# Performance work log

Measured on AMD Instinct MI355X. Metric: run time of the kernel, lower is better.

The kernel has to match this reference:

```python
import jax, jax.numpy as jnp
import numpy as np

FORGET_BIAS = 1.0  # TF BasicLSTMCell default


def lstm_scan(xs, kernel, bias, init_c, init_h):
    """xs: [T, B, D_in]; kernel: [D_in+H, 4H] with TF gate order i, j, f, o."""
    def step(carry, x):
        c, h = carry
        z = jnp.concatenate([x, h], axis=-1) @ kernel + bias  # [B, 4H]
        i, j, f, o = jnp.split(z, 4, axis=-1)
        c_new = c * jax.nn.sigmoid(f + FORGET_BIAS) + jax.nn.sigmoid(i) * jnp.tanh(j)
        h_new = jnp.tanh(c_new) * jax.nn.sigmoid(o)
        return (c_new, h_new), h_new

    (c, h), hs = jax.lax.scan(step, (init_c, init_h), xs)
    return hs, (c, h)


def setup_inputs() -> dict:
    key = jax.random.key(0)
    ks = jax.random.split(key, 8)
    B, T, F = 128, 32, 2048
    H, L, WV, V = 1024, 20, 300, 10000
    s_enc = 1.0 / np.sqrt(F + H)
    s_dec = 1.0 / np.sqrt(WV + H)
    s_prj = 1.0 / np.sqrt(H)
    return {
        "frames": jax.random.normal(ks[0], (B, T, F), jnp.float32),
        "caption": jax.random.randint(ks[1], (B, L), 0, V, jnp.int32),
        "embeddings": jax.random.normal(ks[2], (V, WV), jnp.float32),
        "enc_kernel": jax.random.normal(ks[3], (F + H, 4 * H), jnp.float32) * s_enc,
        "enc_bias": jnp.zeros((4 * H,), jnp.float32),
        "dec_kernel": jax.random.normal(ks[4], (WV + H, 4 * H), jnp.float32) * s_dec,
        "dec_bias": jnp.zeros((4 * H,), jnp.float32),
        "proj_W": jax.random.normal(ks[5], (H, WV), jnp.float32) * s_prj,
        "proj_b": jnp.zeros((WV,), jnp.float32),
    }


def reference(frames, caption, embeddings, enc_kernel, enc_bias,
              dec_kernel, dec_bias, proj_W, proj_b):
    B = frames.shape[0]
    H = proj_W.shape[0]
    # ----- encoder LSTM over video frames -----
    init = (jnp.zeros((B, H), frames.dtype), jnp.zeros((B, H), frames.dtype))
    xs = jnp.swapaxes(frames, 0, 1)  # [T, B, F]
    _, enc_state = lstm_scan(xs, enc_kernel, enc_bias, *init)

    # ----- decoder LSTM with teacher forcing (training branch) -----
    cap_emb = embeddings[caption]                 # [B, L, WV]
    dec_in = jnp.swapaxes(cap_emb, 0, 1)          # [L, B, WV]
    hs, _ = lstm_scan(dec_in, dec_kernel, dec_bias, *enc_state)  # [L, B, H]
    preds = hs @ proj_W + proj_b                  # [L, B, WV]
    return jnp.swapaxes(preds, 0, 1)              # [B, L, WV]
```

## Files before the change

### kernel.cpp

```cpp
#include <hip/hip_runtime.h>
#include <math.h>

#define B_ 128
#define T_ 32
#define F_ 2048
#define H_ 1024
#define L_ 20
#define WV_ 300
#define WVP_ 320
#define NPJ_ 384

typedef unsigned short u16;
typedef unsigned int u32;
typedef __attribute__((ext_vector_type(8))) short bf16x8;
typedef __attribute__((ext_vector_type(4))) float f32x4;

__device__ __forceinline__ u16 f2bf(float x) {
    union { float f; u32 u; } v; v.f = x;
    return (u16)((v.u + 0x7FFFu + ((v.u >> 16) & 1u)) >> 16);
}
__device__ __forceinline__ float bf2f(u16 x) {
    union { u32 u; float f; } v; v.u = ((u32)x) << 16; return v.f;
}
__device__ __forceinline__ void split3(float x, u16& h, u16& m, u16& l) {
    h = f2bf(x);  float r1 = x - bf2f(h);
    m = f2bf(r1); float r2 = r1 - bf2f(m);
    l = f2bf(r2);
}
__device__ __forceinline__ float sigf(float x) { return 1.0f / (1.0f + expf(-x)); }

__device__ __forceinline__ void g2lds16(const void* g, void* l) {
    __builtin_amdgcn_global_load_lds((const __attribute__((address_space(1))) void*)g,
                                     (__attribute__((address_space(3))) void*)l, 16, 0, 0);
}

__device__ __forceinline__ bf16x8 fragld(const u16* tile, int rbase, int lane) {
    int r = rbase + (lane & 15);
    int byte = r * 64 + ((((lane >> 4) ^ (r >> 1)) & 3) << 4);
    return *(const bf16x8*)((const char*)tile + byte);
}

__device__ __forceinline__ void stage_tile(const u16* src, int row_stride, int k0,
                                           u16* lds, int s) {
    int row = s >> 2;
    int ch = (s & 3) ^ ((row >> 1) & 3);
    g2lds16(src + (size_t)row * row_stride + k0 + ch * 8, lds + (size_t)s * 8);
}

template<int MODE_C>
__global__ __launch_bounds__(256)
void gemm6_tn(int M, int N, int K, int Nreal, int NB,
              const u16* __restrict__ A, int lda, size_t aps,
              const u16* __restrict__ Bt, int ldb, size_t bps,
              const float* __restrict__ bias, float* __restrict__ C, int ldc)
{
    __shared__ u16 As[2][3][128 * 32];
    __shared__ u16 Bs[2][3][128 * 32];
    const int tid = threadIdx.x, lane = tid & 63, wid = tid >> 6;
    const int wr = wid >> 1, wc = wid & 1;
    const int bid = blockIdx.x;
    const int bm = (bid / NB) * 128, bn = (bid % NB) * 128;

    f32x4 acc[4][4] = {};
    const u16* Ar = A + (size_t)bm * lda;
    const u16* Br = Bt + (size_t)bn * ldb;

    auto STAGE = [&](int bsel, int k0) {
#pragma unroll
        for (int p = 0; p < 3; ++p) {
            stage_tile(Ar + p * aps, lda, k0, (u16*)As[bsel][p], tid);
            stage_tile(Ar + p * aps, lda, k0, (u16*)As[bsel][p], tid + 256);
            stage_tile(Br + p * bps, ldb, k0, (u16*)Bs[bsel][p], tid);
            stage_tile(Br + p * bps, ldb, k0, (u16*)Bs[bsel][p], tid + 256);
        }
    };

    const int KT = K >> 5;
    STAGE(0, 0);
    __syncthreads();
    for (int kt = 0; kt < KT; ++kt) {
        int pb = kt & 1;
        if (kt + 1 < KT) STAGE(pb ^ 1, (kt + 1) << 5);
        bf16x8 af[3][4];
#pragma unroll
        for (int p = 0; p < 3; ++p)
#pragma unroll
            for (int m = 0; m < 4; ++m) af[p][m] = fragld(As[pb][p], wr * 64 + m * 16, lane);
        {
            bf16x8 bf[4];
#pragma unroll
            for (int n = 0; n < 4; ++n) bf[n] = fragld(Bs[pb][2], wc * 64 + n * 16, lane);
#pragma unroll
            for (int m = 0; m < 4; ++m)
#pragma unroll
                for (int n = 0; n < 4; ++n)
                    acc[m][n] = __builtin_amdgcn_mfma_f32_16x16x32_bf16(af[0][m], bf[n], acc[m][n], 0, 0, 0);
        }
        {
            bf16x8 bf[4];
#pragma unroll
            for (int n = 0; n < 4; ++n) bf[n] = fragld(Bs[pb][1], wc * 64 + n * 16, lane);
#pragma unroll
            for (int m = 0; m < 4; ++m)
#pragma unroll
                for (int n = 0; n < 4; ++n)
                    acc[m][n] = __builtin_amdgcn_mfma_f32_16x16x32_bf16(af[1][m], bf[n], acc[m][n], 0, 0, 0);
#pragma unroll
            for (int m = 0; m < 4; ++m)
#pragma unroll
                for (int n = 0; n < 4; ++n)
                    acc[m][n] = __builtin_amdgcn_mfma_f32_16x16x32_bf16(af[0][m], bf[n], acc[m][n], 0, 0, 0);
        }
        {
            bf16x8 bf[4];
#pragma unroll
            for (int n = 0; n < 4; ++n) bf[n] = fragld(Bs[pb][0], wc * 64 + n * 16, lane);
#pragma unroll
            for (int m = 0; m < 4; ++m)
#pragma unroll
                for (int n = 0; n < 4; ++n)
                    acc[m][n] = __builtin_amdgcn_mfma_f32_16x16x32_bf16(af[2][m], bf[n], acc[m][n], 0, 0, 0);
#pragma unroll
            for (int m = 0; m < 4; ++m)
#pragma unroll
                for (int n = 0; n < 4; ++n)
                    acc[m][n] = __builtin_amdgcn_mfma_f32_16x16x32_bf16(af[1][m], bf[n], acc[m][n], 0, 0, 0);
#pragma unroll
            for (int m = 0; m < 4; ++m)
#pragma unroll
                for (int n = 0; n < 4; ++n)
                    acc[m][n] = __builtin_amdgcn_mfma_f32_16x16x32_bf16(af[0][m], bf[n], acc[m][n], 0, 0, 0);
        }
        __syncthreads();
    }

    const int rq = (lane >> 4) << 2;
    const int cl = lane & 15;
#pragma unroll
    for (int m = 0; m < 4; ++m) {
        int grow = bm + wr * 64 + m * 16 + rq;
#pragma unroll
        for (int n = 0; n < 4; ++n) {
            int gcol = bn + wc * 64 + n * 16 + cl;
            if (gcol < Nreal) {
                float bv = bias ? bias[gcol] : 0.0f;
#pragma unroll
                for (int r = 0; r < 4; ++r) {
                    float v = acc[m][n][r] + bv;
                    int rr = grow + r;
                    if (MODE_C == 0) {
                        C[(size_t)rr * ldc + gcol] = v;
                    } else {
                        int l = rr >> 7, b = rr & 127;
                        C[((size_t)b * L_ + l) * WV_ + gcol] = v;
                    }
                }
            }
        }
    }
}

__global__ __launch_bounds__(256)
void lstm_step6(const u16* __restrict__ hp,
                const u16* __restrict__ WhT,
                const float* __restrict__ xz,
                float* __restrict__ c,
                u16* __restrict__ hop,
                u16* __restrict__ hsp)
{
    const size_t HP = 128 * 1024, WHP = (size_t)4096 * 1024, HSP = (size_t)2560 * 1024;
    __shared__ u16 stg[2][18432];
    __shared__ float zs[32 * 68];
    const int tid = threadIdx.x, lane = tid & 63, w = tid >> 6;
    const int ht = blockIdx.x & 63, q = blockIdx.x >> 6;
    const int r0 = q * 32;
    const int h0 = ht * 16;

    f32x4 acc[2] = {};

    auto STAGE = [&](int bsel, int k0) {
        u16* dstb = &stg[bsel][0];
#pragma unroll
        for (int j = 0; j < 9; ++j) {
            int s = tid + j * 256;
            int sub = s / 1152;
            int s2 = s - sub * 1152;
            int kk = k0 + sub * 32;
            u16* dst = dstb + s * 8;
            if (s2 < 384) {
                int p = s2 >> 7, l = s2 & 127, row = l >> 2;
                int ch = (l & 3) ^ ((row >> 1) & 3);
                g2lds16(hp + (size_t)p * HP + (size_t)(r0 + row) * 1024 + kk + ch * 8, dst);
            } else {
                int t2 = s2 - 384;
                int p = t2 >> 8, l = t2 & 255, row = l >> 2;
                int ch = (l & 3) ^ ((row >> 1) & 3);
                int wrow = (row >> 4) * 1024 + h0 + (row & 15);
                g2lds16(WhT + (size_t)p * WHP + (size_t)wrow * 1024 + kk + ch * 8, dst);
            }
        }
    };

    STAGE(0, 0);
    __syncthreads();
    for (int t = 0; t < 16; ++t) {
        int pb = t & 1;
        if (t < 15) STAGE(pb ^ 1, (t + 1) * 64);
#pragma unroll
        for (int sub = 0; sub < 2; ++sub) {
            const u16* sb = &stg[pb][sub * 9216];
            bf16x8 a[3][2], bfr[3];
#pragma unroll
            for (int p = 0; p < 3; ++p) {
#pragma unroll
                for (int m = 0; m < 2; ++m) a[p][m] = fragld(sb + p * 1024, m * 16, lane);
                bfr[p] = fragld(sb + 3072 + p * 2048, w * 16, lane);
            }
#pragma unroll
            for (int m = 0; m < 2; ++m) acc[m] = __builtin_amdgcn_mfma_f32_16x16x32_bf16(a[0][m], bfr[2], acc[m], 0, 0, 0);
#pragma unroll
            for (int m = 0; m < 2; ++m) acc[m] = __builtin_amdgcn_mfma_f32_16x16x32_bf16(a[1][m], bfr[1], acc[m], 0, 0, 0);
#pragma unroll
            for (int m = 0; m < 2; ++m) acc[m] = __builtin_amdgcn_mfma_f32_16x16x32_bf16(a[0][m], bfr[1], acc[m], 0, 0, 0);
#pragma unroll
            for (int m = 0; m < 2; ++m) acc[m] = __builtin_amdgcn_mfma_f32_16x16x32_bf16(a[2][m], bfr[0], acc[m], 0, 0, 0);
#pragma unroll
            for (int m = 0; m < 2; ++m) acc[m] = __builtin_amdgcn_mfma_f32_16x16x32_bf16(a[1][m], bfr[0], acc[m], 0, 0, 0);
#pragma unroll
            for (int m = 0; m < 2; ++m) acc[m] = __builtin_amdgcn_mfma_f32_16x16x32_bf16(a[0][m], bfr[0], acc[m], 0, 0, 0);
        }
        __syncthreads();
    }

    {
        int zr = (lane >> 4) << 2;
        int zc = lane & 15;
#pragma unroll
        for (int m = 0; m < 2; ++m)
#pragma unroll
            for (int r = 0; r < 4; ++r)
                zs[(m * 16 + zr + r) * 68 + w * 16 + zc] = acc[m][r];
    }
    __syncthreads();

    {
        int row = tid >> 3;
        int cp = (tid & 7) * 2;
        int b = r0 + row;
        int h = h0 + cp;
        const float* xzr = xz + (size_t)b * 4096;
        float2 zi = *(const float2*)&zs[row * 68 + 0  + cp];
        float2 zj = *(const float2*)&zs[row * 68 + 16 + cp];
        float2 zf = *(const float2*)&zs[row * 68 + 32 + cp];
        float2 zo = *(const float2*)&zs[row * 68 + 48 + cp];
        float2 xi = *(const float2*)(xzr + h);
        float2 xj = *(const float2*)(xzr + 1024 + h);
        float2 xf = *(const float2*)(xzr + 2048 + h);
        float2 xo = *(const float2*)(xzr + 3072 + h);
        float2 cv = *(const float2*)(c + (size_t)b * 1024 + h);
        float zia[2] = {zi.x, zi.y}, zja[2] = {zj.x, zj.y};
        float zfa[2] = {zf.x, zf.y}, zoa[2] = {zo.x, zo.y};
        float xia[2] = {xi.x, xi.y}, xja[2] = {xj.x, xj.y};
        float xfa[2] = {xf.x, xf.y}, xoa[2] = {xo.x, xo.y};
        float cva[2] = {cv.x, cv.y};
        float cn[2];
        u16 ph[2], pm[2], pl[2];
#pragma unroll
        for (int e = 0; e < 2; ++e) {
            float i_ = zia[e] + xia[e];
            float j_ = zja[e] + xja[e];
            float f_ = zfa[e] + xfa[e];
            float o_ = zoa[e] + xoa[e];
            float cc = cva[e] * sigf(f_ + 1.0f) + sigf(i_) * tanhf(j_);
            cn[e] = cc;
            float hn = tanhf(cc) * sigf(o_);
            split3(hn, ph[e], pm[e], pl[e]);
        }
        *(float2*)(c + (size_t)b * 1024 + h) = make_float2(cn[0], cn[1]);
        size_t o = (size_t)b * 1024 + h;
        u32 vh = (u32)ph[0] | ((u32)ph[1] << 16);
        u32 vm = (u32)pm[0] | ((u32)pm[1] << 16);
        u32 vl = (u32)pl[0] | ((u32)pl[1] << 16);
        *(u32*)(hop + o) = vh;
        *(u32*)(hop + HP + o) = vm;
        *(u32*)(hop + 2 * HP + o) = vl;
        if (hsp) {
            *(u32*)(hsp + o) = vh;
            *(u32*)(hsp + HSP + o) = vm;
            *(u32*)(hsp + 2 * HSP + o) = vl;
        }
    }
}

__global__ __launch_bounds__(256)
void transpose_split(const float* __restrict__ in, int ldin, int in_row0,
                     int K_in, int N_in, u16* __restrict__ out, int ldout, size_t ps)
{
    __shared__ float tl[32][33];
    const int tid = threadIdx.x;
    const int k0 = blockIdx.x * 32, n0 = blockIdx.y * 32;
    const int cc = tid & 31, rr = tid >> 5;
#pragma unroll
    for (int p = 0; p < 4; ++p) {
        int r = rr + p * 8;
        int k = k0 + r, n = n0 + cc;
        tl[r][cc] = (k < K_in && n < N_in) ? in[(size_t)(in_row0 + k) * ldin + n] : 0.0f;
    }
    __syncthreads();
#pragma unroll
    for (int p = 0; p < 4; ++p) {
        int nr = rr + p * 8;
        u16 h, m, l; split3(tl[cc][nr], h, m, l);
        size_t o = (size_t)(n0 + nr) * ldout + k0 + cc;
        out[o] = h; out[o + ps] = m; out[o + 2 * ps] = l;
    }
}

__global__ __launch_bounds__(256)
void split_frames(const float* __restrict__ fr, int t0, u16* __restrict__ out, size_t ps)
{
    int row = blockIdx.x;
    int t = t0 + (row >> 7), b = row & 127;
    const float* src = fr + ((size_t)b * T_ + t) * F_;
    int off = threadIdx.x * 8;
    float4 v0 = *(const float4*)(src + off);
    float4 v1 = *(const float4*)(src + off + 4);
    float x[8] = {v0.x, v0.y, v0.z, v0.w, v1.x, v1.y, v1.z, v1.w};
    u16 h[8], m[8], l[8];
#pragma unroll
    for (int q = 0; q < 8; ++q) split3(x[q], h[q], m[q], l[q]);
    size_t o = (size_t)row * F_ + off;
    uint4 vh = make_uint4((u32)h[0] | ((u32)h[1] << 16), (u32)h[2] | ((u32)h[3] << 16),
                          (u32)h[4] | ((u32)h[5] << 16), (u32)h[6] | ((u32)h[7] << 16));
    uint4 vm = make_uint4((u32)m[0] | ((u32)m[1] << 16), (u32)m[2] | ((u32)m[3] << 16),
                          (u32)m[4] | ((u32)m[5] << 16), (u32)m[6] | ((u32)m[7] << 16));
    uint4 vl = make_uint4((u32)l[0] | ((u32)l[1] << 16), (u32)l[2] | ((u32)l[3] << 16),
                          (u32)l[4] | ((u32)l[5] << 16), (u32)l[6] | ((u32)l[7] << 16));
    *(uint4*)(out + o) = vh;
    *(uint4*)(out + ps + o) = vm;
    *(uint4*)(out + 2 * ps + o) = vl;
}

__global__ __launch_bounds__(256)
void gather_split(const int* __restrict__ cap, const float* __restrict__ emb,
                  u16* __restrict__ out, size_t ps)
{
    int idx = blockIdx.x * 256 + threadIdx.x;
    if (idx >= 2560 * WVP_) return;
    int v = idx % WVP_;
    int r = idx / WVP_;
    int l = r >> 7, b = r & 127;
    float val = (v < WV_) ? emb[(size_t)cap[b * L_ + l] * WV_ + v] : 0.0f;
    u16 h, m, ll; split3(val, h, m, ll);
    out[idx] = h; out[idx + ps] = m; out[idx + 2 * ps] = ll;
}

extern "C" void kernel_launch(void* const* d_in, const int* in_sizes, int n_in,
                              void* d_out, int out_size, void* d_ws, size_t ws_size,
                              hipStream_t stream)
{
    (void)in_sizes; (void)n_in; (void)out_size; (void)ws_size;
    const float* frames     = (const float*)d_in[0];
    const int*   caption    = (const int*)d_in[1];
    const float* embeddings = (const float*)d_in[2];
    const float* enc_kernel = (const float*)d_in[3];
    const float* enc_bias   = (const float*)d_in[4];
    const float* dec_kernel = (const float*)d_in[5];
    const float* dec_bias   = (const float*)d_in[6];
    const float* proj_W     = (const float*)d_in[7];
    const float* proj_b     = (const float*)d_in[8];
    float* out = (float*)d_out;

    char* base = (char*)d_ws;
    const size_t M1 = 1 << 20;
    const size_t WHP = (size_t)4096 * 1024;
    const size_t ACHP = (size_t)1024 * 2048;
    const size_t WXEP = (size_t)4096 * 2048;
    const size_t WXDP = (size_t)4096 * 320;
    const size_t DECP = (size_t)2560 * 320;
    const size_t WPP  = (size_t)384 * 1024;
    const size_t HSP  = (size_t)2560 * 1024;
    const size_t HBP  = (size_t)128 * 1024;

    float* XZ  = (float*)(base);
    u16* WhE   = (u16*)(base + 16 * M1);
    u16* ACH   = (u16*)(base + 40 * M1);
    u16* WXE   = (u16*)(base + 52 * M1);
    u16* WhD   = (u16*)(base + 52 * M1);
    u16* WXD   = (u16*)((char*)WhD + 3 * WHP * 2);
    u16* DECIN = (u16*)((char*)WXD + 3 * WXDP * 2);
    u16* WP    = (u16*)((char*)DECIN + 3 * DECP * 2);
    u16* HS    = (u16*)(base + 100 * M1);
    u16* HB0   = (u16*)(base + 115 * M1);
    u16* HB1   = (u16*)((char*)HB0 + 3 * HBP * 2);
    float* CB  = (float*)((char*)HB1 + 3 * HBP * 2);

    transpose_split<<<dim3(64, 128), 256, 0, stream>>>(enc_kernel, 4096, 0, 2048, 4096, WXE, 2048, WXEP);
    transpose_split<<<dim3(32, 128), 256, 0, stream>>>(enc_kernel, 4096, 2048, 1024, 4096, WhE, 1024, WHP);
    hipMemsetAsync(CB, 0, HBP * 4, stream);
    hipMemsetAsync(HB0, 0, 3 * HBP * 2, stream);

    u16* hb[2] = { HB0, HB1 };
    int cur = 0;

    for (int ch = 0; ch < 4; ++ch) {
        split_frames<<<1024, 256, 0, stream>>>(frames, ch * 8, ACH, ACHP);
        gemm6_tn<0><<<256, 256, 0, stream>>>(1024, 4096, 2048, 4096, 32,
            ACH, 2048, ACHP, WXE, 2048, WXEP, enc_bias, XZ, 4096);
        for (int tt = 0; tt < 8; ++tt) {
            lstm_step6<<<256, 256, 0, stream>>>(hb[cur], WhE, XZ + (size_t)tt * 128 * 4096,
                CB, hb[cur ^ 1], (u16*)nullptr);
            cur ^= 1;
        }
    }

    transpose_split<<<dim3(32, 128), 256, 0, stream>>>(dec_kernel, 4096, 300, 1024, 4096, WhD, 1024, WHP);
    transpose_split<<<dim3(10, 128), 256, 0, stream>>>(dec_kernel, 4096, 0, 300, 4096, WXD, 320, WXDP);
    transpose_split<<<dim3(32, 12), 256, 0, stream>>>(proj_W, 300, 0, 1024, 300, WP, 1024, WPP);
    gather_split<<<(2560 * WVP_ + 255) / 256, 256, 0, stream>>>(caption, embeddings, DECIN, DECP);

    int l = 0;
    for (int ch = 0; ch < 3; ++ch) {
        int nl = (ch == 2) ? 4 : 8;
        gemm6_tn<0><<<nl * 32, 256, 0, stream>>>(nl * 128, 4096, 320, 4096, 32,
            DECIN + (size_t)ch * 1024 * 320, 320, DECP, WXD, 320, WXDP, dec_bias, XZ, 4096);
        for (int q = 0; q < nl; ++q, ++l) {
            lstm_step6<<<256, 256, 0, stream>>>(hb[cur], WhD, XZ + (size_t)q * 128 * 4096,
                CB, hb[cur ^ 1], HS + (size_t)l * 128 * 1024);
            cur ^= 1;
        }
    }

    gemm6_tn<1><<<60, 256, 0, stream>>>(2560, NPJ_, 1024, 300, 3,
        HS, 1024, HSP, WP, 1024, WPP, proj_b, out, 0);
}
```

Measured before the change: 1.788 ms.

## Halve LSTM step tile width to double blocks, add 3-pass projection GEMM

```diff
diff --git a/kernel.cpp b/kernel.cpp
--- a/kernel.cpp
+++ b/kernel.cpp
@@ -47,15 +47,16 @@
     g2lds16(src + (size_t)row * row_stride + k0 + ch * 8, lds + (size_t)s * 8);
 }
 
-template<int MODE_C>
+template<int MODE_C, int NPASS>
 __global__ __launch_bounds__(256)
 void gemm6_tn(int M, int N, int K, int Nreal, int NB,
               const u16* __restrict__ A, int lda, size_t aps,
               const u16* __restrict__ Bt, int ldb, size_t bps,
               const float* __restrict__ bias, float* __restrict__ C, int ldc)
 {
-    __shared__ u16 As[2][3][128 * 32];
-    __shared__ u16 Bs[2][3][128 * 32];
+    constexpr int NP = (NPASS == 6) ? 3 : 2;
+    __shared__ u16 As[2][NP][128 * 32];
+    __shared__ u16 Bs[2][NP][128 * 32];
     const int tid = threadIdx.x, lane = tid & 63, wid = tid >> 6;
     const int wr = wid >> 1, wc = wid & 1;
     const int bid = blockIdx.x;
@@ -67,7 +68,7 @@
 
     auto STAGE = [&](int bsel, int k0) {
 #pragma unroll
-        for (int p = 0; p < 3; ++p) {
+        for (int p = 0; p < NP; ++p) {
             stage_tile(Ar + p * aps, lda, k0, (u16*)As[bsel][p], tid);
             stage_tile(Ar + p * aps, lda, k0, (u16*)As[bsel][p], tid + 256);
             stage_tile(Br + p * bps, ldb, k0, (u16*)Bs[bsel][p], tid);
@@ -81,15 +82,32 @@
     for (int kt = 0; kt < KT; ++kt) {
         int pb = kt & 1;
         if (kt + 1 < KT) STAGE(pb ^ 1, (kt + 1) << 5);
-        bf16x8 af[3][4];
-#pragma unroll
-        for (int p = 0; p < 3; ++p)
+        bf16x8 af[NP][4];
+#pragma unroll
+        for (int p = 0; p < NP; ++p)
 #pragma unroll
             for (int m = 0; m < 4; ++m) af[p][m] = fragld(As[pb][p], wr * 64 + m * 16, lane);
+        if constexpr (NPASS == 6) {
+            bf16x8 bf[4];
+#pragma unroll
+            for (int n = 0; n < 4; ++n) bf[n] = fragld(Bs[pb][2], wc * 64 + n * 16, lane);
+#pragma unroll
+            for (int m = 0; m < 4; ++m)
+#pragma unroll
+                for (int n = 0; n < 4; ++n)
+                    acc[m][n] = __builtin_amdgcn_mfma_f32_16x16x32_bf16(af[0][m], bf[n], acc[m][n], 0, 0, 0);
+        }
         {
             bf16x8 bf[4];
 #pragma unroll
-            for (int n = 0; n < 4; ++n) bf[n] = fragld(Bs[pb][2], wc * 64 + n * 16, lane);
+            for (int n = 0; n < 4; ++n) bf[n] = fragld(Bs[pb][1], wc * 64 + n * 16, lane);
+            if constexpr (NPASS == 6) {
+#pragma unroll
+                for (int m = 0; m < 4; ++m)
+#pragma unroll
+                    for (int n = 0; n < 4; ++n)
+                        acc[m][n] = __builtin_amdgcn_mfma_f32_16x16x32_bf16(af[1][m], bf[n], acc[m][n], 0, 0, 0);
+            }
 #pragma unroll
             for (int m = 0; m < 4; ++m)
 #pragma unroll
@@ -99,27 +117,14 @@
         {
             bf16x8 bf[4];
 #pragma unroll
-            for (int n = 0; n < 4; ++n) bf[n] = fragld(Bs[pb][1], wc * 64 + n * 16, lane);
-#pragma unroll
-            for (int m = 0; m < 4; ++m)
-#pragma unroll
-                for (int n = 0; n < 4; ++n)
-                    acc[m][n] = __builtin_amdgcn_mfma_f32_16x16x32_bf16(af[1][m], bf[n], acc[m][n], 0, 0, 0);
-#pragma unroll
-            for (int m = 0; m < 4; ++m)
-#pragma unroll
-                for (int n = 0; n < 4; ++n)
-                    acc[m][n] = __builtin_amdgcn_mfma_f32_16x16x32_bf16(af[0][m], bf[n], acc[m][n], 0, 0, 0);
-        }
-        {
-            bf16x8 bf[4];
-#pragma unroll
             for (int n = 0; n < 4; ++n) bf[n] = fragld(Bs[pb][0], wc * 64 + n * 16, lane);
-#pragma unroll
-            for (int m = 0; m < 4; ++m)
-#pragma unroll
-                for (int n = 0; n < 4; ++n)
-                    acc[m][n] = __builtin_amdgcn_mfma_f32_16x16x32_bf16(af[2][m], bf[n], acc[m][n], 0, 0, 0);
+            if constexpr (NPASS == 6) {
+#pragma unroll
+                for (int m = 0; m < 4; ++m)
+#pragma unroll
+                    for (int n = 0; n < 4; ++n)
+                        acc[m][n] = __builtin_amdgcn_mfma_f32_16x16x32_bf16(af[2][m], bf[n], acc[m][n], 0, 0, 0);
+            }
 #pragma unroll
             for (int m = 0; m < 4; ++m)
 #pragma unroll
@@ -169,22 +174,22 @@
                 u16* __restrict__ hsp)
 {
     const size_t HP = 128 * 1024, WHP = (size_t)4096 * 1024, HSP = (size_t)2560 * 1024;
-    __shared__ u16 stg[2][18432];
-    __shared__ float zs[32 * 68];
+    __shared__ u16 stg[2][12288];
+    __shared__ float zs[32 * 36];
     const int tid = threadIdx.x, lane = tid & 63, w = tid >> 6;
-    const int ht = blockIdx.x & 63, q = blockIdx.x >> 6;
+    const int ht = blockIdx.x & 127, q = blockIdx.x >> 7;
     const int r0 = q * 32;
-    const int h0 = ht * 16;
-
-    f32x4 acc[2] = {};
+    const int h0 = ht * 8;
+
+    f32x4 acc = {};
 
     auto STAGE = [&](int bsel, int k0) {
         u16* dstb = &stg[bsel][0];
 #pragma unroll
-        for (int j = 0; j < 9; ++j) {
+        for (int j = 0; j < 6; ++j) {
             int s = tid + j * 256;
-            int sub = s / 1152;
-            int s2 = s - sub * 1152;
+            int sub = (s >= 768) ? 1 : 0;
+            int s2 = s - sub * 768;
             int kk = k0 + sub * 32;
             u16* dst = dstb + s * 8;
             if (s2 < 384) {
@@ -193,13 +198,16 @@
                 g2lds16(hp + (size_t)p * HP + (size_t)(r0 + row) * 1024 + kk + ch * 8, dst);
             } else {
                 int t2 = s2 - 384;
-                int p = t2 >> 8, l = t2 & 255, row = l >> 2;
+                int p = t2 >> 7, l = t2 & 127, row = l >> 2;
                 int ch = (l & 3) ^ ((row >> 1) & 3);
-                int wrow = (row >> 4) * 1024 + h0 + (row & 15);
+                int wrow = (row >> 3) * 1024 + h0 + (row & 7);
                 g2lds16(WhT + (size_t)p * WHP + (size_t)wrow * 1024 + kk + ch * 8, dst);
             }
         }
     };
+
+    const int mrow = (w >> 1) * 16;
+    const int nrow = (w & 1) * 16;
 
     STAGE(0, 0);
     __syncthreads();
@@ -208,87 +216,51 @@
         if (t < 15) STAGE(pb ^ 1, (t + 1) * 64);
 #pragma unroll
         for (int sub = 0; sub < 2; ++sub) {
-            const u16* sb = &stg[pb][sub * 9216];
-            bf16x8 a[3][2], bfr[3];
+            const u16* sb = &stg[pb][sub * 6144];
+            bf16x8 a[3], bfr[3];
 #pragma unroll
             for (int p = 0; p < 3; ++p) {
-#pragma unroll
-                for (int m = 0; m < 2; ++m) a[p][m] = fragld(sb + p * 1024, m * 16, lane);
-                bfr[p] = fragld(sb + 3072 + p * 2048, w * 16, lane);
+                a[p] = fragld(sb + p * 1024, mrow, lane);
+                bfr[p] = fragld(sb + 3072 + p * 1024, nrow, lane);
             }
-#pragma unroll
-            for (int m = 0; m < 2; ++m) acc[m] = __builtin_amdgcn_mfma_f32_16x16x32_bf16(a[0][m], bfr[2], acc[m], 0, 0, 0);
-#pragma unroll
-            for (int m = 0; m < 2; ++m) acc[m] = __builtin_amdgcn_mfma_f32_16x16x32_bf16(a[1][m], bfr[1], acc[m], 0, 0, 0);
-#pragma unroll
-            for (int m = 0; m < 2; ++m) acc[m] = __builtin_amdgcn_mfma_f32_16x16x32_bf16(a[0][m], bfr[1], acc[m], 0, 0, 0);
-#pragma unroll
-            for (int m = 0; m < 2; ++m) acc[m] = __builtin_amdgcn_mfma_f32_16x16x32_bf16(a[2][m], bfr[0], acc[m], 0, 0, 0);
-#pragma unroll
-            for (int m = 0; m < 2; ++m) acc[m] = __builtin_amdgcn_mfma_f32_16x16x32_bf16(a[1][m], bfr[0], acc[m], 0, 0, 0);
-#pragma unroll
-            for (int m = 0; m < 2; ++m) acc[m] = __builtin_amdgcn_mfma_f32_16x16x32_bf16(a[0][m], bfr[0], acc[m], 0, 0, 0);
+            acc = __builtin_amdgcn_mfma_f32_16x16x32_bf16(a[0], bfr[2], acc, 0, 0, 0);
+            acc = __builtin_amdgcn_mfma_f32_16x16x32_bf16(a[1], bfr[1], acc, 0, 0, 0);
+            acc = __builtin_amdgcn_mfma_f32_16x16x32_bf16(a[0], bfr[1], acc, 0, 0, 0);
+            acc = __builtin_amdgcn_mfma_f32_16x16x32_bf16(a[2], bfr[0], acc, 0, 0, 0);
+            acc = __builtin_amdgcn_mfma_f32_16x16x32_bf16(a[1], bfr[0], acc, 0, 0, 0);
+            acc = __builtin_amdgcn_mfma_f32_16x16x32_bf16(a[0], bfr[0], acc, 0, 0, 0);
         }
         __syncthreads();
     }
 
     {
-        int zr = (lane >> 4) << 2;
-        int zc = lane & 15;
-#pragma unroll
-        for (int m = 0; m < 2; ++m)
-#pragma unroll
-            for (int r = 0; r < 4; ++r)
-                zs[(m * 16 + zr + r) * 68 + w * 16 + zc] = acc[m][r];
+        int zr = (w >> 1) * 16 + ((lane >> 4) << 2);
+        int zc = (w & 1) * 16 + (lane & 15);
+#pragma unroll
+        for (int r = 0; r < 4; ++r)
+            zs[(zr + r) * 36 + zc] = acc[r];
     }
     __syncthreads();
 
     {
         int row = tid >> 3;
-        int cp = (tid & 7) * 2;
+        int hc = tid & 7;
         int b = r0 + row;
-        int h = h0 + cp;
+        int h = h0 + hc;
         const float* xzr = xz + (size_t)b * 4096;
-        float2 zi = *(const float2*)&zs[row * 68 + 0  + cp];
-        float2 zj = *(const float2*)&zs[row * 68 + 16 + cp];
-        float2 zf = *(const float2*)&zs[row * 68 + 32 + cp];
-        float2 zo = *(const float2*)&zs[row * 68 + 48 + cp];
-        float2 xi = *(const float2*)(xzr + h);
-        float2 xj = *(const float2*)(xzr + 1024 + h);
-        float2 xf = *(const float2*)(xzr + 2048 + h);
-        float2 xo = *(const float2*)(xzr + 3072 + h);
-        float2 cv = *(const float2*)(c + (size_t)b * 1024 + h);
-        float zia[2] = {zi.x, zi.y}, zja[2] = {zj.x, zj.y};
-        float zfa[2] = {zf.x, zf.y}, zoa[2] = {zo.x, zo.y};
-        float xia[2] = {xi.x, xi.y}, xja[2] = {xj.x, xj.y};
-        float xfa[2] = {xf.x, xf.y}, xoa[2] = {xo.x, xo.y};
-        float cva[2] = {cv.x, cv.y};
-        float cn[2];
-        u16 ph[2], pm[2], pl[2];
-#pragma unroll
-        for (int e = 0; e < 2; ++e) {
-            float i_ = zia[e] + xia[e];
-            float j_ = zja[e] + xja[e];
-            float f_ = zfa[e] + xfa[e];
-            float o_ = zoa[e] + xoa[e];
-            float cc = cva[e] * sigf(f_ + 1.0f) + sigf(i_) * tanhf(j_);
-            cn[e] = cc;
-            float hn = tanhf(cc) * sigf(o_);
-            split3(hn, ph[e], pm[e], pl[e]);
-        }
-        *(float2*)(c + (size_t)b * 1024 + h) = make_float2(cn[0], cn[1]);
+        float zi = zs[row * 36 + 0  + hc] + xzr[h];
+        float zj = zs[row * 36 + 8  + hc] + xzr[1024 + h];
+        float zf = zs[row * 36 + 16 + hc] + xzr[2048 + h];
+        float zo = zs[row * 36 + 24 + hc] + xzr[3072 + h];
+        float cv = c[(size_t)b * 1024 + h];
+        float cc = cv * sigf(zf + 1.0f) + sigf(zi) * tanhf(zj);
+        float hn = tanhf(cc) * sigf(zo);
+        u16 ph, pm, pl;
+        split3(hn, ph, pm, pl);
+        c[(size_t)b * 1024 + h] = cc;
         size_t o = (size_t)b * 1024 + h;
-        u32 vh = (u32)ph[0] | ((u32)ph[1] << 16);
-        u32 vm = (u32)pm[0] | ((u32)pm[1] << 16);
-        u32 vl = (u32)pl[0] | ((u32)pl[1] << 16);
-        *(u32*)(hop + o) = vh;
-        *(u32*)(hop + HP + o) = vm;
-        *(u32*)(hop + 2 * HP + o) = vl;
-        if (hsp) {
-            *(u32*)(hsp + o) = vh;
-            *(u32*)(hsp + HSP + o) = vm;
-            *(u32*)(hsp + 2 * HSP + o) = vl;
-        }
+        hop[o] = ph; hop[HP + o] = pm; hop[2 * HP + o] = pl;
+        if (hsp) { hsp[o] = ph; hsp[HSP + o] = pm; hsp[2 * HSP + o] = pl; }
     }
 }
 
@@ -405,10 +377,10 @@
 
     for (int ch = 0; ch < 4; ++ch) {
         split_frames<<<1024, 256, 0, stream>>>(frames, ch * 8, ACH, ACHP);
-        gemm6_tn<0><<<256, 256, 0, stream>>>(1024, 4096, 2048, 4096, 32,
+        gemm6_tn<0, 6><<<256, 256, 0, stream>>>(1024, 4096, 2048, 4096, 32,
             ACH, 2048, ACHP, WXE, 2048, WXEP, enc_bias, XZ, 4096);
         for (int tt = 0; tt < 8; ++tt) {
-            lstm_step6<<<256, 256, 0, stream>>>(hb[cur], WhE, XZ + (size_t)tt * 128 * 4096,
+            lstm_step6<<<512, 256, 0, stream>>>(hb[cur], WhE, XZ + (size_t)tt * 128 * 4096,
                 CB, hb[cur ^ 1], (u16*)nullptr);
             cur ^= 1;
         }
@@ -422,15 +394,15 @@
     int l = 0;
     for (int ch = 0; ch < 3; ++ch) {
         int nl = (ch == 2) ? 4 : 8;
-        gemm6_tn<0><<<nl * 32, 256, 0, stream>>>(nl * 128, 4096, 320, 4096, 32,
+        gemm6_tn<0, 6><<<nl * 32, 256, 0, stream>>>(nl * 128, 4096, 320, 4096, 32,
             DECIN + (size_t)ch * 1024 * 320, 320, DECP, WXD, 320, WXDP, dec_bias, XZ, 4096);
         for (int q = 0; q < nl; ++q, ++l) {
-            lstm_step6<<<256, 256, 0, stream>>>(hb[cur], WhD, XZ + (size_t)q * 128 * 4096,
+            lstm_step6<<<512, 256, 0, stream>>>(hb[cur], WhD, XZ + (size_t)q * 128 * 4096,
                 CB, hb[cur ^ 1], HS + (size_t)l * 128 * 1024);
             cur ^= 1;
         }
     }
 
-    gemm6_tn<1><<<60, 256, 0, stream>>>(2560, NPJ_, 1024, 300, 3,
+    gemm6_tn<1, 3><<<60, 256, 0, stream>>>(2560, NPJ_, 1024, 300, 3,
         HS, 1024, HSP, WP, 1024, WPP, proj_b, out, 0);
 }
```

After: 1.631 ms. 8.8% less time.
